# Performance work log

Hardware: AMD Instinct MI355X
Metric: run time of the kernel (lower is better)

## Reference

```python
import jax, jax.numpy as jnp
import numpy as np

SCALE = 64.0
MARGIN = 0.35
EPS = 1e-12  # torch F.normalize eps


def _l2norm(a, axis):
    n = jnp.sqrt(jnp.sum(a * a, axis=axis, keepdims=True))
    return a / jnp.maximum(n, EPS)


def setup_inputs() -> dict:
    key = jax.random.key(0)
    k1, k2, k3 = jax.random.split(key, 3)
    B, D, C = 512, 512, 100000
    x = jax.random.normal(k1, (B, D), dtype=jnp.float32)
    gt = jax.random.randint(k2, (B,), 0, C, dtype=jnp.int64)
    # kaiming_normal_ on [C, D]: std = sqrt(2 / fan_in) with fan_in = D
    wt = jax.random.normal(k3, (C, D), dtype=jnp.float32) * np.sqrt(2.0 / D)
    return {"x": x, "gt": gt, "wt": wt}


def reference(x, gt, wt):
    wt_norm = _l2norm(wt, axis=1)          # [C, D]
    x_norm = _l2norm(x, axis=1)            # [B, D]
    cos = jnp.einsum("bd,cd->bc", x_norm, wt_norm)  # [B, C]
    # margin only at target index (avoids materializing one-hot)
    b = jnp.arange(x.shape[0])
    margin_score = cos.at[b, gt].add(-MARGIN)
    logits = SCALE * margin_score
    logp = jax.nn.log_softmax(logits, axis=-1)
    nll = -logp[b, gt]
    return jnp.mean(nll)
```

## Files before the change

kernel.cpp:

```cpp
#include <hip/hip_runtime.h>
#include <hip/hip_bf16.h>

#define DIM 512
#define BATCH 512
#define CCLS 100000
#define BM 256
#define BN 128
#define NT 782

typedef __attribute__((ext_vector_type(4))) float f32x4;
typedef __attribute__((ext_vector_type(4))) int i32x4;
typedef __attribute__((ext_vector_type(8))) int i32x8;

__device__ __forceinline__ void async_copy16(const unsigned char* g, unsigned char* l) {
  __builtin_amdgcn_global_load_lds((const __attribute__((address_space(1))) void*)g,
                                   (__attribute__((address_space(3))) void*)l, 16, 0, 0);
}

__global__ __launch_bounds__(256) void rownorm_fp8(const float* __restrict__ wt,
                                                   const float* __restrict__ x,
                                                   unsigned char* __restrict__ wn,
                                                   unsigned char* __restrict__ xn) {
  int wave = threadIdx.x >> 6;
  int lane = threadIdx.x & 63;
  int row4 = blockIdx.x * 4 + wave;
  const float* in;
  unsigned char* out;
  int row;
  if (row4 < CCLS) { in = wt; out = wn; row = row4; }
  else             { in = x;  out = xn; row = row4 - CCLS; }
  const float4* src = (const float4*)(in + (size_t)row * DIM);
  float4 v0 = src[2 * lane];
  float4 v1 = src[2 * lane + 1];
  float ss = v0.x*v0.x + v0.y*v0.y + v0.z*v0.z + v0.w*v0.w
           + v1.x*v1.x + v1.y*v1.y + v1.z*v1.z + v1.w*v1.w;
  #pragma unroll
  for (int off = 32; off > 0; off >>= 1) ss += __shfl_xor(ss, off, 64);
  float r = 1.0f / fmaxf(sqrtf(ss), 1e-12f);
  int p0 = __builtin_amdgcn_cvt_pk_fp8_f32(v0.x * r, v0.y * r, 0, false);
  p0     = __builtin_amdgcn_cvt_pk_fp8_f32(v0.z * r, v0.w * r, p0, true);
  int p1 = __builtin_amdgcn_cvt_pk_fp8_f32(v1.x * r, v1.y * r, 0, false);
  p1     = __builtin_amdgcn_cvt_pk_fp8_f32(v1.z * r, v1.w * r, p1, true);
  ((int2*)(out + (size_t)row * DIM))[lane] = make_int2(p0, p1);
}

__global__ __launch_bounds__(512, 2) void cosface_gemm(
    const unsigned char* __restrict__ xn,
    const unsigned char* __restrict__ wn,
    const int* __restrict__ gt,
    float* __restrict__ partial,
    float* __restrict__ tgt) {
  __shared__ __align__(16) unsigned char lds_a[2][BM * 128];
  __shared__ __align__(16) unsigned char lds_b[2][BN * 128];
  __shared__ float lds_rowsum[BM];
  __shared__ int lds_gt[BM];

  const int tid = threadIdx.x;
  const int lane = tid & 63;
  const int w = tid >> 6;
  const int wm = w >> 1;
  const int wn_ = w & 1;
  const int mt = blockIdx.x;
  const int nt = blockIdx.y;

  if (tid < BM) {
    lds_rowsum[tid] = 0.f;
    lds_gt[tid] = gt[mt * BM + tid];
  }

  unsigned int oa[4];
  unsigned int ob[2];
  #pragma unroll
  for (int j = 0; j < 4; ++j) {
    int c = j * 512 + tid;
    int m = c >> 3;
    int qg = (c & 7) ^ (m & 7);
    oa[j] = (unsigned int)(mt * BM + m) * DIM + qg * 16;
  }
  #pragma unroll
  for (int j = 0; j < 2; ++j) {
    int c = j * 512 + tid;
    int m = c >> 3;
    int qg = (c & 7) ^ (m & 7);
    int rowB = nt * BN + m;
    if (rowB >= CCLS) rowB = CCLS - 1;
    ob[j] = (unsigned int)rowB * DIM + qg * 16;
  }

#define STAGE(sel, kk) do {                                                  \
    _Pragma("unroll")                                                        \
    for (int j = 0; j < 4; ++j)                                              \
      async_copy16(xn + oa[j] + (kk) * 128, &lds_a[sel][(j * 512 + w * 64) * 16]); \
    _Pragma("unroll")                                                        \
    for (int j = 0; j < 2; ++j)                                              \
      async_copy16(wn + ob[j] + (kk) * 128, &lds_b[sel][(j * 512 + w * 64) * 16]); \
  } while (0)

  f32x4 acc[4][4];
  #pragma unroll
  for (int i = 0; i < 4; ++i)
    #pragma unroll
    for (int j = 0; j < 4; ++j)
      acc[i][j] = (f32x4){0.f, 0.f, 0.f, 0.f};

  const int quad = lane >> 4;
  const int l15 = lane & 15;
  const int arow = wm * 64 + l15;
  const int brow = wn_ * 64 + l15;
  const int swA = arow & 7;
  const int swB = brow & 7;
  const int c0 = quad * 2;
  const int c1 = quad * 2 + 1;

  STAGE(0, 0);
  __syncthreads();

  #pragma unroll
  for (int kk = 0; kk < 4; ++kk) {
    const int cur = kk & 1;
    if (kk < 3) STAGE(cur ^ 1, kk + 1);

    i32x8 af[4];
    #pragma unroll
    for (int i = 0; i < 4; ++i) {
      const unsigned char* pa = &lds_a[cur][(arow + i * 16) * 128];
      i32x4 lo = *(const i32x4*)(pa + ((c0 ^ swA) << 4));
      i32x4 hi = *(const i32x4*)(pa + ((c1 ^ swA) << 4));
      af[i] = __builtin_shufflevector(lo, hi, 0, 1, 2, 3, 4, 5, 6, 7);
    }
    #pragma unroll
    for (int j = 0; j < 4; ++j) {
      const unsigned char* pb = &lds_b[cur][(brow + j * 16) * 128];
      i32x4 lo = *(const i32x4*)(pb + ((c0 ^ swB) << 4));
      i32x4 hi = *(const i32x4*)(pb + ((c1 ^ swB) << 4));
      i32x8 bf = __builtin_shufflevector(lo, hi, 0, 1, 2, 3, 4, 5, 6, 7);
      #pragma unroll
      for (int i = 0; i < 4; ++i)
        acc[i][j] = __builtin_amdgcn_mfma_scale_f32_16x16x128_f8f6f4(
            af[i], bf, acc[i][j], 0, 0, 0, 127, 0, 127);
    }

    if (kk < 3) {
      asm volatile("s_waitcnt vmcnt(0)" ::: "memory");
      __builtin_amdgcn_s_barrier();
      asm volatile("" ::: "memory");
    }
  }
#undef STAGE

  #pragma unroll
  for (int i = 0; i < 4; ++i) {
    #pragma unroll
    for (int reg = 0; reg < 4; ++reg) {
      int m_loc = wm * 64 + i * 16 + quad * 4 + reg;
      int m_g = mt * BM + m_loc;
      int gtm = lds_gt[m_loc];
      float s = 0.f;
      #pragma unroll
      for (int j = 0; j < 4; ++j) {
        int n_g = nt * BN + wn_ * 64 + j * 16 + l15;
        float logit = 64.f * acc[i][j][reg];
        if (n_g == gtm) {
          logit -= 64.f * 0.35f;
          tgt[m_g] = logit;
        }
        if (n_g < CCLS) s += __expf(logit - 64.f);
      }
      #pragma unroll
      for (int off = 1; off < 16; off <<= 1) s += __shfl_xor(s, off, 64);
      if (l15 == 0) atomicAdd(&lds_rowsum[m_loc], s);
    }
  }
  __syncthreads();
  if (tid < BM)
    partial[(size_t)(mt * BM + tid) * NT + nt] = lds_rowsum[tid];
}

__global__ __launch_bounds__(64) void nll_rows(const float* __restrict__ partial,
                                               const float* __restrict__ tgt,
                                               float* __restrict__ nll) {
  int m = blockIdx.x;
  int lane = threadIdx.x;
  const float* row = partial + (size_t)m * NT;
  float s = 0.f;
  for (int t = lane; t < NT; t += 64) s += row[t];
  #pragma unroll
  for (int off = 32; off > 0; off >>= 1) s += __shfl_xor(s, off, 64);
  if (lane == 0) nll[m] = (logf(s) + 64.f) - tgt[m];
}

__global__ __launch_bounds__(512) void reduce_mean(const float* __restrict__ nll,
                                                   float* __restrict__ out) {
  __shared__ float red[BATCH];
  int m = threadIdx.x;
  red[m] = nll[m];
  __syncthreads();
  for (int k = 256; k > 0; k >>= 1) {
    if (m < k) red[m] += red[m + k];
    __syncthreads();
  }
  if (m == 0) out[0] = red[0] * (1.0f / BATCH);
}

extern "C" void kernel_launch(void* const* d_in, const int* in_sizes, int n_in,
                              void* d_out, int out_size, void* d_ws, size_t ws_size,
                              hipStream_t stream) {
  const float* x  = (const float*)d_in[0];
  const int*   gt = (const int*)d_in[1];
  const float* wt = (const float*)d_in[2];
  float* out = (float*)d_out;

  char* ws = (char*)d_ws;
  unsigned char* wn = (unsigned char*)ws;
  unsigned char* xn = (unsigned char*)(ws + 51200000);
  float* partial    = (float*)(ws + 51462144);
  float* tgt        = (float*)(ws + 53063680);
  float* nll        = (float*)(ws + 53065728);

  rownorm_fp8<<<(CCLS + BATCH) / 4, 256, 0, stream>>>(wt, x, wn, xn);
  cosface_gemm<<<dim3(2, NT), 512, 0, stream>>>(xn, wn, gt, partial, tgt);
  nll_rows<<<BATCH, 64, 0, stream>>>(partial, tgt, nll);
  reduce_mean<<<1, BATCH, 0, stream>>>(nll, out);
}
```

Measured before the change: 361.9 us.

## Halve GEMM M-tile, flatten grid with XCD-aware block remap

```diff
diff --git a/kernel.cpp b/kernel.cpp
--- a/kernel.cpp
+++ b/kernel.cpp
@@ -4,8 +4,9 @@
 #define DIM 512
 #define BATCH 512
 #define CCLS 100000
-#define BM 256
+#define BM 128
 #define BN 128
+#define MT 4
 #define NT 782
 
 typedef __attribute__((ext_vector_type(4))) float f32x4;
@@ -44,7 +45,7 @@
   ((int2*)(out + (size_t)row * DIM))[lane] = make_int2(p0, p1);
 }
 
-__global__ __launch_bounds__(512, 2) void cosface_gemm(
+__global__ __launch_bounds__(512, 4) void cosface_gemm(
     const unsigned char* __restrict__ xn,
     const unsigned char* __restrict__ wn,
     const int* __restrict__ gt,
@@ -58,30 +59,27 @@
   const int tid = threadIdx.x;
   const int lane = tid & 63;
   const int w = tid >> 6;
-  const int wm = w >> 1;
-  const int wn_ = w & 1;
-  const int mt = blockIdx.x;
-  const int nt = blockIdx.y;
+  const int wm = w >> 2;
+  const int wn_ = w & 3;
+
+  int flat = blockIdx.x;
+  int f = (flat & 7) * 391 + (flat >> 3);
+  const int mt = f & 3;
+  const int nt = f >> 2;
 
   if (tid < BM) {
     lds_rowsum[tid] = 0.f;
     lds_gt[tid] = gt[mt * BM + tid];
   }
 
-  unsigned int oa[4];
+  unsigned int oa[2];
   unsigned int ob[2];
   #pragma unroll
-  for (int j = 0; j < 4; ++j) {
+  for (int j = 0; j < 2; ++j) {
     int c = j * 512 + tid;
     int m = c >> 3;
     int qg = (c & 7) ^ (m & 7);
     oa[j] = (unsigned int)(mt * BM + m) * DIM + qg * 16;
-  }
-  #pragma unroll
-  for (int j = 0; j < 2; ++j) {
-    int c = j * 512 + tid;
-    int m = c >> 3;
-    int qg = (c & 7) ^ (m & 7);
     int rowB = nt * BN + m;
     if (rowB >= CCLS) rowB = CCLS - 1;
     ob[j] = (unsigned int)rowB * DIM + qg * 16;
@@ -89,26 +87,23 @@
 
 #define STAGE(sel, kk) do {                                                  \
     _Pragma("unroll")                                                        \
-    for (int j = 0; j < 4; ++j)                                              \
+    for (int j = 0; j < 2; ++j)                                              \
       async_copy16(xn + oa[j] + (kk) * 128, &lds_a[sel][(j * 512 + w * 64) * 16]); \
     _Pragma("unroll")                                                        \
     for (int j = 0; j < 2; ++j)                                              \
       async_copy16(wn + ob[j] + (kk) * 128, &lds_b[sel][(j * 512 + w * 64) * 16]); \
   } while (0)
 
-  f32x4 acc[4][4];
+  f32x4 acc[4][2];
   #pragma unroll
   for (int i = 0; i < 4; ++i)
     #pragma unroll
-    for (int j = 0; j < 4; ++j)
+    for (int j = 0; j < 2; ++j)
       acc[i][j] = (f32x4){0.f, 0.f, 0.f, 0.f};
 
   const int quad = lane >> 4;
   const int l15 = lane & 15;
-  const int arow = wm * 64 + l15;
-  const int brow = wn_ * 64 + l15;
-  const int swA = arow & 7;
-  const int swB = brow & 7;
+  const int sw = l15 & 7;
   const int c0 = quad * 2;
   const int c1 = quad * 2 + 1;
 
@@ -120,24 +115,24 @@
     const int cur = kk & 1;
     if (kk < 3) STAGE(cur ^ 1, kk + 1);
 
-    i32x8 af[4];
+    i32x8 bf[2];
+    #pragma unroll
+    for (int j = 0; j < 2; ++j) {
+      const unsigned char* pb = &lds_b[cur][(wn_ * 32 + j * 16 + l15) * 128];
+      i32x4 lo = *(const i32x4*)(pb + ((c0 ^ sw) << 4));
+      i32x4 hi = *(const i32x4*)(pb + ((c1 ^ sw) << 4));
+      bf[j] = __builtin_shufflevector(lo, hi, 0, 1, 2, 3, 4, 5, 6, 7);
+    }
     #pragma unroll
     for (int i = 0; i < 4; ++i) {
-      const unsigned char* pa = &lds_a[cur][(arow + i * 16) * 128];
-      i32x4 lo = *(const i32x4*)(pa + ((c0 ^ swA) << 4));
-      i32x4 hi = *(const i32x4*)(pa + ((c1 ^ swA) << 4));
-      af[i] = __builtin_shufflevector(lo, hi, 0, 1, 2, 3, 4, 5, 6, 7);
-    }
-    #pragma unroll
-    for (int j = 0; j < 4; ++j) {
-      const unsigned char* pb = &lds_b[cur][(brow + j * 16) * 128];
-      i32x4 lo = *(const i32x4*)(pb + ((c0 ^ swB) << 4));
-      i32x4 hi = *(const i32x4*)(pb + ((c1 ^ swB) << 4));
-      i32x8 bf = __builtin_shufflevector(lo, hi, 0, 1, 2, 3, 4, 5, 6, 7);
+      const unsigned char* pa = &lds_a[cur][(wm * 64 + i * 16 + l15) * 128];
+      i32x4 lo = *(const i32x4*)(pa + ((c0 ^ sw) << 4));
+      i32x4 hi = *(const i32x4*)(pa + ((c1 ^ sw) << 4));
+      i32x8 af = __builtin_shufflevector(lo, hi, 0, 1, 2, 3, 4, 5, 6, 7);
       #pragma unroll
-      for (int i = 0; i < 4; ++i)
+      for (int j = 0; j < 2; ++j)
         acc[i][j] = __builtin_amdgcn_mfma_scale_f32_16x16x128_f8f6f4(
-            af[i], bf, acc[i][j], 0, 0, 0, 127, 0, 127);
+            af, bf[j], acc[i][j], 0, 0, 0, 127, 0, 127);
     }
 
     if (kk < 3) {
@@ -157,8 +152,8 @@
       int gtm = lds_gt[m_loc];
       float s = 0.f;
       #pragma unroll
-      for (int j = 0; j < 4; ++j) {
-        int n_g = nt * BN + wn_ * 64 + j * 16 + l15;
+      for (int j = 0; j < 2; ++j) {
+        int n_g = nt * BN + wn_ * 32 + j * 16 + l15;
         float logit = 64.f * acc[i][j][reg];
         if (n_g == gtm) {
           logit -= 64.f * 0.35f;
@@ -218,7 +213,7 @@
   float* nll        = (float*)(ws + 53065728);
 
   rownorm_fp8<<<(CCLS + BATCH) / 4, 256, 0, stream>>>(wt, x, wn, xn);
-  cosface_gemm<<<dim3(2, NT), 512, 0, stream>>>(xn, wn, gt, partial, tgt);
+  cosface_gemm<<<MT * NT, 512, 0, stream>>>(xn, wn, gt, partial, tgt);
   nll_rows<<<BATCH, 64, 0, stream>>>(partial, tgt, nll);
   reduce_mean<<<1, BATCH, 0, stream>>>(nll, out);
 }
```

After: 501.6 us. +38.6%, slower.
